# Kernel tuning notes

Measured on AMD Instinct MI355X. Metric: run time of the kernel, lower is better.

The kernel has to match this reference:

```python
import jax, jax.numpy as jnp
import numpy as np
from jax import lax
from jax.scipy.special import logsumexp

B, T, K = 512, 1024, 64


def _numerator(emissions, tags, maskf, start, end, trans):
    # score of the gold path, matching torchcrf._compute_score
    b = jnp.arange(emissions.shape[0])
    s = start[tags[:, 0]] + emissions[b, 0, tags[:, 0]]                      # [B]
    trans_sc = trans[tags[:, :-1], tags[:, 1:]]                               # [B,T-1]
    em_sc = jnp.take_along_axis(emissions, tags[..., None], axis=2)[..., 0]   # [B,T]
    s = s + jnp.sum((trans_sc + em_sc[:, 1:]) * maskf[:, 1:], axis=1)
    seq_ends = maskf.sum(axis=1).astype(jnp.int32) - 1                        # [B]
    last_tags = tags[b, seq_ends]
    return s + end[last_tags]


def _log_norm(emissions, mask, start, end, trans):
    # forward algorithm (log partition), matching torchcrf._compute_normalizer
    alpha0 = start[None, :] + emissions[:, 0]                                 # [B,K]

    def step(alpha, inp):
        em_t, m_t = inp                                                       # [B,K], [B]
        nxt = logsumexp(alpha[:, :, None] + trans[None] + em_t[:, None, :], axis=1)
        alpha = jnp.where(m_t[:, None], nxt, alpha)
        return alpha, None

    alpha, _ = lax.scan(step, alpha0,
                        (emissions[:, 1:].transpose(1, 0, 2), mask[:, 1:].T))
    return logsumexp(alpha + end[None, :], axis=1)                            # [B]


def _viterbi(emissions, mask, start, end, trans):
    # Viterbi decode, matching torchcrf._viterbi_decode (padded to [B,T])
    Bn = emissions.shape[0]
    score0 = start[None, :] + emissions[:, 0]                                 # [B,K]

    def step(score, inp):
        em_t, m_t = inp
        cand = score[:, :, None] + trans[None]                                # [B,K,K]
        best_prev = jnp.argmax(cand, axis=1).astype(jnp.int32)                # [B,K]
        nxt = jnp.max(cand, axis=1) + em_t
        score = jnp.where(m_t[:, None], nxt, score)
        return score, best_prev

    score, history = lax.scan(step, score0,
                              (emissions[:, 1:].transpose(1, 0, 2), mask[:, 1:].T))
    last = jnp.argmax(score + end[None, :], axis=1).astype(jnp.int32)         # [B]
    barange = jnp.arange(Bn)

    def back(idx, inp):
        hist_t, m_t = inp                                                     # [B,K], [B]
        prev = hist_t[barange, idx]
        idx = jnp.where(m_t, prev, idx)
        return idx, idx

    _, early = lax.scan(back, last, (history, mask[:, 1:].T), reverse=True)   # [T-1,B]
    return jnp.concatenate([early.T, last[:, None]], axis=1)                  # [B,T]


def setup_inputs() -> dict:
    key = jax.random.key(0)
    k1, k2, k3, k4, k5 = jax.random.split(key, 5)
    emissions = jax.random.normal(k1, (B, T, K), dtype=jnp.float32)
    attn_mask = jnp.ones((B, T), dtype=bool)
    tags = jax.random.randint(k2, (B, T), 0, K)
    start_transitions = 0.1 * jax.random.normal(k3, (K,), dtype=jnp.float32)
    end_transitions = 0.1 * jax.random.normal(k4, (K,), dtype=jnp.float32)
    transitions = 0.1 * jax.random.normal(k5, (K, K), dtype=jnp.float32)
    return {"emissions": emissions, "attn_mask": attn_mask, "tags": tags,
            "start_transitions": start_transitions,
            "end_transitions": end_transitions, "transitions": transitions}


def reference(emissions, attn_mask, tags, start_transitions, end_transitions, transitions):
    mask = attn_mask.astype(bool)
    maskf = mask.astype(emissions.dtype)
    decode = _viterbi(emissions, mask, start_transitions, end_transitions, transitions)
    num = _numerator(emissions, tags, maskf, start_transitions, end_transitions, transitions)
    logz = _log_norm(emissions, mask, start_transitions, end_transitions, transitions)
    loss = -(num - logz)  # crf(..., reduction='none').neg()
    return (decode, loss)
```

## Files before the change

### kernel.cpp

```cpp
#include <hip/hip_runtime.h>

#define CB 512
#define CT 1024
#define CK 64
#define LOG2E 1.44269504088896340736f
#define LN2   0.69314718055994530942f
#define VSC   512.0f

typedef short sh2 __attribute__((ext_vector_type(2)));
typedef float v2f __attribute__((ext_vector_type(2)));

__device__ __forceinline__ sh2 as_sh2(int x) { union { int i; sh2 v; } u; u.i = x; return u.v; }
__device__ __forceinline__ float rlf(float v, int l) {
  return __int_as_float(__builtin_amdgcn_readlane(__float_as_int(v), l));
}

template <bool FOLD>
__device__ __forceinline__ int vit_step_reg(
    int S, int kn, const sh2* tpk2, float em_t, unsigned char* hrow)
{
  int sw[32];
  #pragma unroll
  for (int q = 0; q < 32; ++q) {
    int lo = __builtin_amdgcn_readlane(S, 2 * q);
    int hi = __builtin_amdgcn_readlane(S, 2 * q + 1);
    sw[q] = (lo & 0xffff) | (hi << 16);
  }
  sh2 aa[16];
  #pragma unroll
  for (int j = 0; j < 16; ++j)
    aa[j] = __builtin_elementwise_max(as_sh2(sw[2 * j]) + tpk2[2 * j],
                                      as_sh2(sw[2 * j + 1]) + tpk2[2 * j + 1]);
  #pragma unroll
  for (int st = 8; st; st >>= 1)
    #pragma unroll
    for (int j = 0; j < st; ++j)
      aa[j] = __builtin_elementwise_max(aa[j], aa[j + st]);
  int vmax = max((int)aa[0].x, (int)aa[0].y);
  int S0 = (int)(short)sw[0];

  hrow[kn] = (unsigned char)(vmax & 63);

  if (FOLD) {
    float em2 = em_t * LOG2E;
    return (((vmax & ~63) - S0) + (int)(em2 * VSC)) & ~63;
  }
  return ((vmax & ~63) - S0) & ~63;
}

template <bool FOLD>
__device__ __forceinline__ float sum_step_reg(
    float V, const v2f* wv, float em_t, float& Macc)
{
  float V0 = rlf(V, 0);
  float r  = __builtin_amdgcn_rcpf(V0);
  Macc -= __builtin_amdgcn_logf(r);

  v2f acc0 = {0.f, 0.f}, acc1 = {0.f, 0.f}, acc2 = {0.f, 0.f}, acc3 = {0.f, 0.f};
  #pragma unroll
  for (int q = 0; q < 32; q += 4) {
    v2f b0 = { rlf(V, 2 * q),     rlf(V, 2 * q + 1) };
    v2f b1 = { rlf(V, 2 * q + 2), rlf(V, 2 * q + 3) };
    v2f b2 = { rlf(V, 2 * q + 4), rlf(V, 2 * q + 5) };
    v2f b3 = { rlf(V, 2 * q + 6), rlf(V, 2 * q + 7) };
    acc0 = __builtin_elementwise_fma(b0, wv[q],     acc0);
    acc1 = __builtin_elementwise_fma(b1, wv[q + 1], acc1);
    acc2 = __builtin_elementwise_fma(b2, wv[q + 2], acc2);
    acc3 = __builtin_elementwise_fma(b3, wv[q + 3], acc3);
  }
  v2f avt = (acc0 + acc1) + (acc2 + acc3);
  float ssum = avt.x + avt.y;

  if (FOLD) {
    float em2 = em_t * LOG2E;
    return (ssum * r) * __builtin_amdgcn_exp2f(em2);
  }
  return ssum * r;
}

__global__ __launch_bounds__(512, 4) void crf_fused(
    const float* __restrict__ em,
    const int*   __restrict__ tags,
    const float* __restrict__ startt,
    const float* __restrict__ endt,
    const float* __restrict__ trans,
    float* __restrict__ out)
{
  const int b   = blockIdx.x;
  const int tid = threadIdx.x;
  const int kn  = tid & 63;
  const int g   = tid >> 6;

  extern __shared__ char smem[];
  int*   SSa1 = (int*)smem;
  int*   SSb1 = SSa1 + 32;
  float* VVa1 = (float*)(SSb1 + 32);
  float* VVb1 = VVa1 + 64;
  float* fsh  = VVb1 + 64;
  float* mish = fsh + 8;
  unsigned char* hist = (unsigned char*)(smem + 3200);
  unsigned char* bmap = hist + CT * CK;
  unsigned char* path = bmap + 4096;
  unsigned char* bnd  = path + 1024;

  const float* emb = em + (size_t)b * (CT * CK);

  if (g < 4) {
    sh2 tpk2[32];
    const int fwd = (g < 2);
    #pragma unroll
    for (int q = 0; q < 32; ++q) {
      int jA = 2 * q, jB = 2 * q + 1;
      float trA = fwd ? trans[jA * CK + kn] : trans[kn * CK + jA];
      float trB = fwd ? trans[jB * CK + kn] : trans[kn * CK + jB];
      float tA2 = trA * LOG2E, tB2 = trB * LOG2E;
      sh2 t; t.x = (short)((((int)(tA2 * VSC)) & ~63) | jA);
             t.y = (short)((((int)(tB2 * VSC)) & ~63) | jB);
      tpk2[q] = t;
    }
    if (g == 0) {
      float ref0 = LOG2E * (startt[0] + emb[0]);
      float a0   = LOG2E * (startt[kn] + emb[kn]);
      int S = ((int)((a0 - ref0) * VSC)) & ~63;
      float ef1 = emb[64 + kn], ef2 = emb[128 + kn], ef3 = emb[192 + kn];
      int pf = (4 << 6) + kn;
      unsigned char* hr = hist + 64;
      #pragma unroll 1
      for (int t = 0; t < 287; ++t) {
        float emt = ef1; ef1 = ef2; ef2 = ef3; ef3 = emb[pf]; pf += 64;
        S = vit_step_reg<true>(S, kn, tpk2, emt, hr); hr += 64;
      }
    } else if (g == 1) {
      float e0 = emb[(223 << 6)];
      int S = ((int)(((emb[(223 << 6) + kn] - e0) * LOG2E) * VSC)) & ~63;
      float ef1 = emb[(224 << 6) + kn], ef2 = emb[(225 << 6) + kn], ef3 = emb[(226 << 6) + kn];
      int pf = (227 << 6) + kn;
      #pragma unroll 1
      for (int t = 0; t < 64; ++t) {
        float emt = ef1; ef1 = ef2; ef2 = ef3; ef3 = emb[pf]; pf += 64;
        S = vit_step_reg<true>(S, kn, tpk2, emt, hist);
      }
      unsigned char* hr = hist + (288 << 6);
      #pragma unroll 1
      for (int t = 0; t < 224; ++t) {
        float emt = ef1; ef1 = ef2; ef2 = ef3; ef3 = emb[pf]; pf += 64;
        S = vit_step_reg<true>(S, kn, tpk2, emt, hr); hr += 64;
      }
      ((short*)SSa1)[kn] = (short)S;
    } else if (g == 2) {
      const float* emL = emb + 1023 * CK;
      float refb = LOG2E * (endt[0] + emL[0]);
      float b0   = LOG2E * (endt[kn] + emL[kn]);
      int S = ((int)((b0 - refb) * VSC)) & ~63;
      float eb1 = emb[(1022 << 6) + kn], eb2 = emb[(1021 << 6) + kn], eb3 = emb[(1020 << 6) + kn];
      int pfB = (1019 << 6) + kn;
      unsigned char* hrB = hist + (1023 << 6);
      #pragma unroll 1
      for (int t = 0; t < 288; ++t) {
        float emt = eb1; eb1 = eb2; eb2 = eb3; eb3 = emb[pfB]; pfB -= 64;
        S = vit_step_reg<true>(S, kn, tpk2, emt, hrB); hrB -= 64;
      }
    } else {
      float e0 = emb[(799 << 6)];
      int S = ((int)(((emb[(799 << 6) + kn] - e0) * LOG2E) * VSC)) & ~63;
      float eb1 = emb[(798 << 6) + kn], eb2 = emb[(797 << 6) + kn], eb3 = emb[(796 << 6) + kn];
      int pfB = (795 << 6) + kn;
      #pragma unroll 1
      for (int t = 0; t < 64; ++t) {
        float emt = eb1; eb1 = eb2; eb2 = eb3; eb3 = emb[pfB]; pfB -= 64;
        S = vit_step_reg<true>(S, kn, tpk2, emt, hist);
      }
      unsigned char* hrB = hist + (735 << 6);
      #pragma unroll 1
      for (int t = 0; t < 223; ++t) {
        float emt = eb1; eb1 = eb2; eb2 = eb3; eb3 = emb[pfB]; pfB -= 64;
        S = vit_step_reg<true>(S, kn, tpk2, emt, hrB); hrB -= 64;
      }
      S = vit_step_reg<false>(S, kn, tpk2, 0.f, hrB);
      ((short*)SSb1)[kn] = (short)S;
    }
  } else {
    v2f wv[32];
    const int fwd = (g < 6);
    #pragma unroll
    for (int q = 0; q < 32; ++q) {
      int jA = 2 * q, jB = 2 * q + 1;
      float trA = fwd ? trans[jA * CK + kn] : trans[kn * CK + jA];
      float trB = fwd ? trans[jB * CK + kn] : trans[kn * CK + jB];
      v2f w2 = {__builtin_amdgcn_exp2f(trA * LOG2E), __builtin_amdgcn_exp2f(trB * LOG2E)};
      wv[q] = w2;
    }
    float Macc;
    if (g == 4) {
      float ref0 = LOG2E * (startt[0] + emb[0]);
      Macc = ref0;
      float V = __builtin_amdgcn_exp2f(LOG2E * (startt[kn] + emb[kn]) - ref0);
      float ef1 = emb[64 + kn], ef2 = emb[128 + kn], ef3 = emb[192 + kn];
      int pf = (4 << 6) + kn;
      #pragma unroll 1
      for (int t = 0; t < 287; ++t) {
        float emt = ef1; ef1 = ef2; ef2 = ef3; ef3 = emb[pf]; pf += 64;
        V = sum_step_reg<true>(V, wv, emt, Macc);
      }
      if (kn == 0) mish[0] = Macc + __builtin_amdgcn_logf(V);
    } else if (g == 5) {
      float e0 = emb[(223 << 6)];
      Macc = 0.f;
      float V = __builtin_amdgcn_exp2f((emb[(223 << 6) + kn] - e0) * LOG2E);
      float ef1 = emb[(224 << 6) + kn], ef2 = emb[(225 << 6) + kn], ef3 = emb[(226 << 6) + kn];
      int pf = (227 << 6) + kn;
      #pragma unroll 1
      for (int t = 0; t < 64; ++t) {
        float emt = ef1; ef1 = ef2; ef2 = ef3; ef3 = emb[pf]; pf += 64;
        V = sum_step_reg<true>(V, wv, emt, Macc);
      }
      Macc = -__builtin_amdgcn_logf(rlf(V, 0));
      #pragma unroll 1
      for (int t = 0; t < 224; ++t) {
        float emt = ef1; ef1 = ef2; ef2 = ef3; ef3 = emb[pf]; pf += 64;
        V = sum_step_reg<true>(V, wv, emt, Macc);
      }
      VVa1[kn] = V;
      if (kn == 0) mish[1] = Macc;
    } else if (g == 6) {
      const float* emL = emb + 1023 * CK;
      float refb = LOG2E * (endt[0] + emL[0]);
      Macc = refb;
      float V = __builtin_amdgcn_exp2f(LOG2E * (endt[kn] + emL[kn]) - refb);
      float eb1 = emb[(1022 << 6) + kn], eb2 = emb[(1021 << 6) + kn], eb3 = emb[(1020 << 6) + kn];
      int pfB = (1019 << 6) + kn;
      #pragma unroll 1
      for (int t = 0; t < 288; ++t) {
        float emt = eb1; eb1 = eb2; eb2 = eb3; eb3 = emb[pfB]; pfB -= 64;
        V = sum_step_reg<true>(V, wv, emt, Macc);
      }
      if (kn == 0) mish[2] = Macc + __builtin_amdgcn_logf(V);
    } else {
      float e0 = emb[(799 << 6)];
      Macc = 0.f;
      float V = __builtin_amdgcn_exp2f((emb[(799 << 6) + kn] - e0) * LOG2E);
      float eb1 = emb[(798 << 6) + kn], eb2 = emb[(797 << 6) + kn], eb3 = emb[(796 << 6) + kn];
      int pfB = (795 << 6) + kn;
      #pragma unroll 1
      for (int t = 0; t < 64; ++t) {
        float emt = eb1; eb1 = eb2; eb2 = eb3; eb3 = emb[pfB]; pfB -= 64;
        V = sum_step_reg<true>(V, wv, emt, Macc);
      }
      Macc = -__builtin_amdgcn_logf(rlf(V, 0));
      #pragma unroll 1
      for (int t = 0; t < 223; ++t) {
        float emt = eb1; eb1 = eb2; eb2 = eb3; eb3 = emb[pfB]; pfB -= 64;
        V = sum_step_reg<true>(V, wv, emt, Macc);
      }
      V = sum_step_reg<true>(V, wv, eb1, Macc);
      V = sum_step_reg<false>(V, wv, 0.f, Macc);
      VVb1[kn] = V;
      if (kn == 0) mish[3] = Macc;
    }
  }
  __syncthreads();

  float logz = 0.0f; int last = 0;
  if (tid < 64) {
    int swa = SSa1[(kn >> 1)];
    int swb = SSb1[(kn >> 1)];
    int sa = (kn & 1) ? (swa >> 16) : (int)(short)swa;
    int sb = (kn & 1) ? (swb >> 16) : (int)(short)swb;
    int tot = ((sa + sb) << 6) | kn;
    #pragma unroll
    for (int off = 32; off; off >>= 1) tot = max(tot, __shfl_xor(tot, off));
    last = tot & 63;
    float dd = VVa1[kn] * VVb1[kn];
    #pragma unroll
    for (int off = 32; off; off >>= 1) dd += __shfl_xor(dd, off);
    logz = LN2 * (mish[0] + mish[1] + mish[2] + mish[3] + __builtin_amdgcn_logf(dd));
  }

  float local = 0.0f;
  #pragma unroll
  for (int q = 0; q < 2; ++q) {
    int t  = tid + (q << 9);
    int tg = tags[b * CT + t];
    float e = emb[(t << 6) + tg];
    if (t == 0) local += startt[tg] + e;
    else {
      int tp = tags[b * CT + t - 1];
      local += trans[(tp << 6) + tg] + e;
    }
    if (t == CT - 1) local += endt[tg];
  }
  #pragma unroll
  for (int off = 32; off; off >>= 1) local += __shfl_xor(local, off);
  if (kn == 0) fsh[g] = local;

  int cur[8];
  #pragma unroll
  for (int q = 0; q < 8; ++q) cur[q] = (tid + (q << 9)) & 63;
  #pragma unroll
  for (int idx = 0; idx < 16; ++idx) {
    #pragma unroll
    for (int q = 0; q < 8; ++q) {
      int s = (tid + (q << 9)) >> 6;
      if (s < 63) {
        int row = (s < 31) ? ((s << 4) + 16 - idx) : (512 + ((s - 31) << 4) + idx);
        cur[q] = hist[(row << 6) + cur[q]];
      }
    }
  }
  #pragma unroll
  for (int q = 0; q < 8; ++q) {
    int s = (tid + (q << 9)) >> 6;
    if (s < 63) bmap[(s << 6) + ((tid + (q << 9)) & 63)] = (unsigned char)cur[q];
  }
  __syncthreads();

  if (tid == 0) {
    float num = fsh[0] + fsh[1] + fsh[2] + fsh[3] + fsh[4] + fsh[5] + fsh[6] + fsh[7];
    out[(size_t)CB * CT + b] = logz - num;
    int xx = last;
    for (int t = 511; t > 496; --t) xx = hist[(t << 6) + xx];
    bnd[31] = (unsigned char)xx;
    for (int s = 30; s >= 0; --s) { xx = bmap[(s << 6) + xx]; bnd[s] = (unsigned char)xx; }
    int yy = last;
    bnd[64] = (unsigned char)yy;
    for (int r2 = 0; r2 < 32; ++r2) { yy = bmap[((31 + r2) << 6) + yy]; bnd[64 + r2 + 1] = (unsigned char)yy; }
  }
  __syncthreads();

  if (tid < 64) {
    if (tid < 31) {
      int s = tid; int xx = bnd[s + 1];
      for (int t = (s << 4) + 16; t > (s << 4); --t) { xx = hist[(t << 6) + xx]; path[t - 1] = (unsigned char)xx; }
    } else if (tid == 31) {
      int xx = last;
      path[511] = (unsigned char)xx;
      for (int t = 511; t > 496; --t) { xx = hist[(t << 6) + xx]; path[t - 1] = (unsigned char)xx; }
    } else {
      int r2 = tid - 32; int xx = bnd[64 + r2];
      int base = 512 + (r2 << 4);
      for (int idx = 0; idx < 16; ++idx) { xx = hist[((base + idx) << 6) + xx]; path[base + idx] = (unsigned char)xx; }
    }
  }
  __syncthreads();

  #pragma unroll
  for (int q = 0; q < 2; ++q) {
    int i2 = tid + (q << 9);
    out[(size_t)b * CT + i2] = (float)path[i2];
  }
}

extern "C" void kernel_launch(void* const* d_in, const int* in_sizes, int n_in,
                              void* d_out, int out_size, void* d_ws, size_t ws_size,
                              hipStream_t stream) {
  (void)in_sizes; (void)n_in; (void)d_ws; (void)ws_size; (void)out_size;
  const float* em     = (const float*)d_in[0];
  const int*   tags   = (const int*)d_in[2];
  const float* startt = (const float*)d_in[3];
  const float* endt   = (const float*)d_in[4];
  const float* trans  = (const float*)d_in[5];
  float* out = (float*)d_out;

  const size_t smem = 3200 + 65536 + 4096 + 1024 + 128;
  crf_fused<<<dim3(CB), dim3(512), smem, stream>>>(em, tags, startt, endt, trans, out);
}
```

Measured before the change: 442.8 us.

## Drop mid-sequence split chains; use 4 waves with pre-packed shuffle state

New measurement: 452.0 us. 2.1% more time.

```diff
diff --git a/kernel.cpp b/kernel.cpp
--- a/kernel.cpp
+++ b/kernel.cpp
@@ -8,68 +8,67 @@
 #define VSC   512.0f
 
 typedef short sh2 __attribute__((ext_vector_type(2)));
-typedef float v2f __attribute__((ext_vector_type(2)));
 
 __device__ __forceinline__ sh2 as_sh2(int x) { union { int i; sh2 v; } u; u.i = x; return u.v; }
 __device__ __forceinline__ float rlf(float v, int l) {
   return __int_as_float(__builtin_amdgcn_readlane(__float_as_int(v), l));
 }
 
+__device__ __forceinline__ int pack2(int Sn, int kn) {
+  int lo = __shfl(Sn, (kn & 31) * 2);
+  int hi = __shfl(Sn, (kn & 31) * 2 + 1);
+  return (lo & 0xffff) | (hi << 16);
+}
+
 template <bool FOLD>
-__device__ __forceinline__ int vit_step_reg(
-    int S, int kn, const sh2* tpk2, float em_t, unsigned char* hrow)
+__device__ __forceinline__ int vit_step_rl(
+    int P, int kn, const sh2* tpk2, float em_t, unsigned char* hrow)
 {
-  int sw[32];
-  #pragma unroll
-  for (int q = 0; q < 32; ++q) {
-    int lo = __builtin_amdgcn_readlane(S, 2 * q);
-    int hi = __builtin_amdgcn_readlane(S, 2 * q + 1);
-    sw[q] = (lo & 0xffff) | (hi << 16);
-  }
   sh2 aa[16];
   #pragma unroll
-  for (int j = 0; j < 16; ++j)
-    aa[j] = __builtin_elementwise_max(as_sh2(sw[2 * j]) + tpk2[2 * j],
-                                      as_sh2(sw[2 * j + 1]) + tpk2[2 * j + 1]);
+  for (int j = 0; j < 16; ++j) {
+    int pA = __builtin_amdgcn_readlane(P, 2 * j);
+    int pB = __builtin_amdgcn_readlane(P, 2 * j + 1);
+    aa[j] = __builtin_elementwise_max(as_sh2(pA) + tpk2[2 * j],
+                                      as_sh2(pB) + tpk2[2 * j + 1]);
+  }
   #pragma unroll
   for (int st = 8; st; st >>= 1)
     #pragma unroll
     for (int j = 0; j < st; ++j)
       aa[j] = __builtin_elementwise_max(aa[j], aa[j + st]);
   int vmax = max((int)aa[0].x, (int)aa[0].y);
-  int S0 = (int)(short)sw[0];
+  int S0 = (int)(short)__builtin_amdgcn_readlane(P, 0);
 
   hrow[kn] = (unsigned char)(vmax & 63);
 
+  int Sn;
   if (FOLD) {
     float em2 = em_t * LOG2E;
-    return (((vmax & ~63) - S0) + (int)(em2 * VSC)) & ~63;
-  }
-  return ((vmax & ~63) - S0) & ~63;
+    Sn = (((vmax & ~63) - S0) + (int)(em2 * VSC)) & ~63;
+  } else {
+    Sn = ((vmax & ~63) - S0) & ~63;
+  }
+  return pack2(Sn, kn);
 }
 
 template <bool FOLD>
-__device__ __forceinline__ float sum_step_reg(
-    float V, const v2f* wv, float em_t, float& Macc)
+__device__ __forceinline__ float sum_step_rl(
+    float V, const float* w, float em_t, float& Macc)
 {
   float V0 = rlf(V, 0);
   float r  = __builtin_amdgcn_rcpf(V0);
   Macc -= __builtin_amdgcn_logf(r);
 
-  v2f acc0 = {0.f, 0.f}, acc1 = {0.f, 0.f}, acc2 = {0.f, 0.f}, acc3 = {0.f, 0.f};
-  #pragma unroll
-  for (int q = 0; q < 32; q += 4) {
-    v2f b0 = { rlf(V, 2 * q),     rlf(V, 2 * q + 1) };
-    v2f b1 = { rlf(V, 2 * q + 2), rlf(V, 2 * q + 3) };
-    v2f b2 = { rlf(V, 2 * q + 4), rlf(V, 2 * q + 5) };
-    v2f b3 = { rlf(V, 2 * q + 6), rlf(V, 2 * q + 7) };
-    acc0 = __builtin_elementwise_fma(b0, wv[q],     acc0);
-    acc1 = __builtin_elementwise_fma(b1, wv[q + 1], acc1);
-    acc2 = __builtin_elementwise_fma(b2, wv[q + 2], acc2);
-    acc3 = __builtin_elementwise_fma(b3, wv[q + 3], acc3);
-  }
-  v2f avt = (acc0 + acc1) + (acc2 + acc3);
-  float ssum = avt.x + avt.y;
+  float a0 = 0.f, a1 = 0.f, a2 = 0.f, a3 = 0.f;
+  #pragma unroll
+  for (int j = 0; j < 64; j += 4) {
+    a0 = fmaf(rlf(V, j),     w[j],     a0);
+    a1 = fmaf(rlf(V, j + 1), w[j + 1], a1);
+    a2 = fmaf(rlf(V, j + 2), w[j + 2], a2);
+    a3 = fmaf(rlf(V, j + 3), w[j + 3], a3);
+  }
+  float ssum = (a0 + a1) + (a2 + a3);
 
   if (FOLD) {
     float em2 = em_t * LOG2E;
@@ -78,7 +77,7 @@
   return ssum * r;
 }
 
-__global__ __launch_bounds__(512, 4) void crf_fused(
+__global__ __launch_bounds__(256, 2) void crf_fused(
     const float* __restrict__ em,
     const int*   __restrict__ tags,
     const float* __restrict__ startt,
@@ -97,7 +96,7 @@
   float* VVa1 = (float*)(SSb1 + 32);
   float* VVb1 = VVa1 + 64;
   float* fsh  = VVb1 + 64;
-  float* mish = fsh + 8;
+  float* mish = fsh + 4;
   unsigned char* hist = (unsigned char*)(smem + 3200);
   unsigned char* bmap = hist + CT * CK;
   unsigned char* path = bmap + 4096;
@@ -105,9 +104,9 @@
 
   const float* emb = em + (size_t)b * (CT * CK);
 
-  if (g < 4) {
+  if (g < 2) {
     sh2 tpk2[32];
-    const int fwd = (g < 2);
+    const int fwd = (g == 0);
     #pragma unroll
     for (int q = 0; q < 32; ++q) {
       int jA = 2 * q, jB = 2 * q + 1;
@@ -121,108 +120,55 @@
     if (g == 0) {
       float ref0 = LOG2E * (startt[0] + emb[0]);
       float a0   = LOG2E * (startt[kn] + emb[kn]);
-      int S = ((int)((a0 - ref0) * VSC)) & ~63;
+      int P = pack2(((int)((a0 - ref0) * VSC)) & ~63, kn);
       float ef1 = emb[64 + kn], ef2 = emb[128 + kn], ef3 = emb[192 + kn];
       int pf = (4 << 6) + kn;
       unsigned char* hr = hist + 64;
       #pragma unroll 1
-      for (int t = 0; t < 287; ++t) {
+      for (int t = 0; t < 511; ++t) {
         float emt = ef1; ef1 = ef2; ef2 = ef3; ef3 = emb[pf]; pf += 64;
-        S = vit_step_reg<true>(S, kn, tpk2, emt, hr); hr += 64;
-      }
-    } else if (g == 1) {
-      float e0 = emb[(223 << 6)];
-      int S = ((int)(((emb[(223 << 6) + kn] - e0) * LOG2E) * VSC)) & ~63;
-      float ef1 = emb[(224 << 6) + kn], ef2 = emb[(225 << 6) + kn], ef3 = emb[(226 << 6) + kn];
-      int pf = (227 << 6) + kn;
-      #pragma unroll 1
-      for (int t = 0; t < 64; ++t) {
-        float emt = ef1; ef1 = ef2; ef2 = ef3; ef3 = emb[pf]; pf += 64;
-        S = vit_step_reg<true>(S, kn, tpk2, emt, hist);
-      }
-      unsigned char* hr = hist + (288 << 6);
-      #pragma unroll 1
-      for (int t = 0; t < 224; ++t) {
-        float emt = ef1; ef1 = ef2; ef2 = ef3; ef3 = emb[pf]; pf += 64;
-        S = vit_step_reg<true>(S, kn, tpk2, emt, hr); hr += 64;
-      }
-      ((short*)SSa1)[kn] = (short)S;
-    } else if (g == 2) {
+        P = vit_step_rl<true>(P, kn, tpk2, emt, hr); hr += 64;
+      }
+      if (kn < 32) SSa1[kn] = P;
+    } else {
       const float* emL = emb + 1023 * CK;
       float refb = LOG2E * (endt[0] + emL[0]);
       float b0   = LOG2E * (endt[kn] + emL[kn]);
-      int S = ((int)((b0 - refb) * VSC)) & ~63;
+      int P = pack2(((int)((b0 - refb) * VSC)) & ~63, kn);
       float eb1 = emb[(1022 << 6) + kn], eb2 = emb[(1021 << 6) + kn], eb3 = emb[(1020 << 6) + kn];
       int pfB = (1019 << 6) + kn;
       unsigned char* hrB = hist + (1023 << 6);
       #pragma unroll 1
-      for (int t = 0; t < 288; ++t) {
+      for (int t = 0; t < 511; ++t) {
         float emt = eb1; eb1 = eb2; eb2 = eb3; eb3 = emb[pfB]; pfB -= 64;
-        S = vit_step_reg<true>(S, kn, tpk2, emt, hrB); hrB -= 64;
-      }
-    } else {
-      float e0 = emb[(799 << 6)];
-      int S = ((int)(((emb[(799 << 6) + kn] - e0) * LOG2E) * VSC)) & ~63;
-      float eb1 = emb[(798 << 6) + kn], eb2 = emb[(797 << 6) + kn], eb3 = emb[(796 << 6) + kn];
-      int pfB = (795 << 6) + kn;
-      #pragma unroll 1
-      for (int t = 0; t < 64; ++t) {
-        float emt = eb1; eb1 = eb2; eb2 = eb3; eb3 = emb[pfB]; pfB -= 64;
-        S = vit_step_reg<true>(S, kn, tpk2, emt, hist);
-      }
-      unsigned char* hrB = hist + (735 << 6);
-      #pragma unroll 1
-      for (int t = 0; t < 223; ++t) {
-        float emt = eb1; eb1 = eb2; eb2 = eb3; eb3 = emb[pfB]; pfB -= 64;
-        S = vit_step_reg<true>(S, kn, tpk2, emt, hrB); hrB -= 64;
-      }
-      S = vit_step_reg<false>(S, kn, tpk2, 0.f, hrB);
-      ((short*)SSb1)[kn] = (short)S;
+        P = vit_step_rl<true>(P, kn, tpk2, emt, hrB); hrB -= 64;
+      }
+      P = vit_step_rl<false>(P, kn, tpk2, 0.f, hrB);
+      if (kn < 32) SSb1[kn] = P;
     }
   } else {
-    v2f wv[32];
-    const int fwd = (g < 6);
-    #pragma unroll
-    for (int q = 0; q < 32; ++q) {
-      int jA = 2 * q, jB = 2 * q + 1;
-      float trA = fwd ? trans[jA * CK + kn] : trans[kn * CK + jA];
-      float trB = fwd ? trans[jB * CK + kn] : trans[kn * CK + jB];
-      v2f w2 = {__builtin_amdgcn_exp2f(trA * LOG2E), __builtin_amdgcn_exp2f(trB * LOG2E)};
-      wv[q] = w2;
+    float w[64];
+    const int fwd = (g == 2);
+    #pragma unroll
+    for (int j = 0; j < 64; ++j) {
+      float tr = fwd ? trans[j * CK + kn] : trans[kn * CK + j];
+      w[j] = __builtin_amdgcn_exp2f(tr * LOG2E);
     }
     float Macc;
-    if (g == 4) {
+    if (g == 2) {
       float ref0 = LOG2E * (startt[0] + emb[0]);
       Macc = ref0;
       float V = __builtin_amdgcn_exp2f(LOG2E * (startt[kn] + emb[kn]) - ref0);
       float ef1 = emb[64 + kn], ef2 = emb[128 + kn], ef3 = emb[192 + kn];
       int pf = (4 << 6) + kn;
       #pragma unroll 1
-      for (int t = 0; t < 287; ++t) {
+      for (int t = 0; t < 511; ++t) {
         float emt = ef1; ef1 = ef2; ef2 = ef3; ef3 = emb[pf]; pf += 64;
-        V = sum_step_reg<true>(V, wv, emt, Macc);
-      }
-      if (kn == 0) mish[0] = Macc + __builtin_amdgcn_logf(V);
-    } else if (g == 5) {
-      float e0 = emb[(223 << 6)];
-      Macc = 0.f;
-      float V = __builtin_amdgcn_exp2f((emb[(223 << 6) + kn] - e0) * LOG2E);
-      float ef1 = emb[(224 << 6) + kn], ef2 = emb[(225 << 6) + kn], ef3 = emb[(226 << 6) + kn];
-      int pf = (227 << 6) + kn;
-      #pragma unroll 1
-      for (int t = 0; t < 64; ++t) {
-        float emt = ef1; ef1 = ef2; ef2 = ef3; ef3 = emb[pf]; pf += 64;
-        V = sum_step_reg<true>(V, wv, emt, Macc);
-      }
-      Macc = -__builtin_amdgcn_logf(rlf(V, 0));
-      #pragma unroll 1
-      for (int t = 0; t < 224; ++t) {
-        float emt = ef1; ef1 = ef2; ef2 = ef3; ef3 = emb[pf]; pf += 64;
-        V = sum_step_reg<true>(V, wv, emt, Macc);
+        V = sum_step_rl<true>(V, w, emt, Macc);
       }
       VVa1[kn] = V;
       if (kn == 0) mish[1] = Macc;
-    } else if (g == 6) {
+    } else {
       const float* emL = emb + 1023 * CK;
       float refb = LOG2E * (endt[0] + emL[0]);
       Macc = refb;
@@ -230,32 +176,13 @@
       float eb1 = emb[(1022 << 6) + kn], eb2 = emb[(1021 << 6) + kn], eb3 = emb[(1020 << 6) + kn];
       int pfB = (1019 << 6) + kn;
       #pragma unroll 1
-      for (int t = 0; t < 288; ++t) {
+      for (int t = 0; t < 511; ++t) {
         float emt = eb1; eb1 = eb2; eb2 = eb3; eb3 = emb[pfB]; pfB -= 64;
-        V = sum_step_reg<true>(V, wv, emt, Macc);
-      }
-      if (kn == 0) mish[2] = Macc + __builtin_amdgcn_logf(V);
-    } else {
-      float e0 = emb[(799 << 6)];
-      Macc = 0.f;
-      float V = __builtin_amdgcn_exp2f((emb[(799 << 6) + kn] - e0) * LOG2E);
-      float eb1 = emb[(798 << 6) + kn], eb2 = emb[(797 << 6) + kn], eb3 = emb[(796 << 6) + kn];
-      int pfB = (795 << 6) + kn;
-      #pragma unroll 1
-      for (int t = 0; t < 64; ++t) {
-        float emt = eb1; eb1 = eb2; eb2 = eb3; eb3 = emb[pfB]; pfB -= 64;
-        V = sum_step_reg<true>(V, wv, emt, Macc);
-      }
-      Macc = -__builtin_amdgcn_logf(rlf(V, 0));
-      #pragma unroll 1
-      for (int t = 0; t < 223; ++t) {
-        float emt = eb1; eb1 = eb2; eb2 = eb3; eb3 = emb[pfB]; pfB -= 64;
-        V = sum_step_reg<true>(V, wv, emt, Macc);
-      }
-      V = sum_step_reg<true>(V, wv, eb1, Macc);
-      V = sum_step_reg<false>(V, wv, 0.f, Macc);
+        V = sum_step_rl<true>(V, w, emt, Macc);
+      }
+      V = sum_step_rl<false>(V, w, 0.f, Macc);
       VVb1[kn] = V;
-      if (kn == 0) mish[3] = Macc;
+      if (kn == 0) mish[0] = Macc;
     }
   }
   __syncthreads();
@@ -273,13 +200,13 @@
     float dd = VVa1[kn] * VVb1[kn];
     #pragma unroll
     for (int off = 32; off; off >>= 1) dd += __shfl_xor(dd, off);
-    logz = LN2 * (mish[0] + mish[1] + mish[2] + mish[3] + __builtin_amdgcn_logf(dd));
+    logz = LN2 * (mish[0] + mish[1] + __builtin_amdgcn_logf(dd));
   }
 
   float local = 0.0f;
   #pragma unroll
-  for (int q = 0; q < 2; ++q) {
-    int t  = tid + (q << 9);
+  for (int q = 0; q < 4; ++q) {
+    int t  = tid + (q << 8);
     int tg = tags[b * CT + t];
     float e = emb[(t << 6) + tg];
     if (t == 0) local += startt[tg] + e;
@@ -293,14 +220,14 @@
   for (int off = 32; off; off >>= 1) local += __shfl_xor(local, off);
   if (kn == 0) fsh[g] = local;
 
-  int cur[8];
-  #pragma unroll
-  for (int q = 0; q < 8; ++q) cur[q] = (tid + (q << 9)) & 63;
+  int cur[16];
+  #pragma unroll
+  for (int q = 0; q < 16; ++q) cur[q] = (tid + (q << 8)) & 63;
   #pragma unroll
   for (int idx = 0; idx < 16; ++idx) {
     #pragma unroll
-    for (int q = 0; q < 8; ++q) {
-      int s = (tid + (q << 9)) >> 6;
+    for (int q = 0; q < 16; ++q) {
+      int s = (tid + (q << 8)) >> 6;
       if (s < 63) {
         int row = (s < 31) ? ((s << 4) + 16 - idx) : (512 + ((s - 31) << 4) + idx);
         cur[q] = hist[(row << 6) + cur[q]];
@@ -308,14 +235,14 @@
     }
   }
   #pragma unroll
-  for (int q = 0; q < 8; ++q) {
-    int s = (tid + (q << 9)) >> 6;
-    if (s < 63) bmap[(s << 6) + ((tid + (q << 9)) & 63)] = (unsigned char)cur[q];
+  for (int q = 0; q < 16; ++q) {
+    int s = (tid + (q << 8)) >> 6;
+    if (s < 63) bmap[(s << 6) + ((tid + (q << 8)) & 63)] = (unsigned char)cur[q];
   }
   __syncthreads();
 
   if (tid == 0) {
-    float num = fsh[0] + fsh[1] + fsh[2] + fsh[3] + fsh[4] + fsh[5] + fsh[6] + fsh[7];
+    float num = fsh[0] + fsh[1] + fsh[2] + fsh[3];
     out[(size_t)CB * CT + b] = logz - num;
     int xx = last;
     for (int t = 511; t > 496; --t) xx = hist[(t << 6) + xx];
@@ -344,8 +271,8 @@
   __syncthreads();
 
   #pragma unroll
-  for (int q = 0; q < 2; ++q) {
-    int i2 = tid + (q << 9);
+  for (int q = 0; q < 4; ++q) {
+    int i2 = tid + (q << 8);
     out[(size_t)b * CT + i2] = (float)path[i2];
   }
 }
@@ -362,5 +289,5 @@
   float* out = (float*)d_out;
 
   const size_t smem = 3200 + 65536 + 4096 + 1024 + 128;
-  crf_fused<<<dim3(CB), dim3(512), smem, stream>>>(em, tags, startt, endt, trans, out);
-}
+  crf_fused<<<dim3(CB), dim3(256), smem, stream>>>(em, tags, startt, endt, trans, out);
+}
```
